# Kernel optimization log

Hardware: AMD Instinct MI355X
Metric: run time of the kernel (lower is better)

The kernel has to match this reference:

```python
import jax, jax.numpy as jnp
import numpy as np


def setup_inputs() -> dict:
    key = jax.random.key(0)
    ks = jax.random.split(key, 6)
    B, S, E, H = 8, 2048, 1024, 64
    scale = 1.0 / np.sqrt(E)
    return {
        "query": jax.random.normal(ks[0], (B, S, E), dtype=jnp.float32),
        "key": jax.random.normal(ks[1], (B, S, E), dtype=jnp.float32),
        "value": jax.random.normal(ks[2], (B, S, E), dtype=jnp.float32),
        "Wq": jax.random.normal(ks[3], (E, H), dtype=jnp.float32) * scale,
        "bq": jnp.zeros((H,), dtype=jnp.float32),
        "Wk": jax.random.normal(ks[4], (E, H), dtype=jnp.float32) * scale,
        "bk": jnp.zeros((H,), dtype=jnp.float32),
        "Wv": jax.random.normal(ks[5], (E, H), dtype=jnp.float32) * scale,
        "bv": jnp.zeros((H,), dtype=jnp.float32),
    }


def reference(query, key, value, Wq, bq, Wk, bk, Wv, bv):
    # Linear projections: [B,S,E] @ [E,H] + [H] -> [B,S,H]
    q = jnp.einsum("bse,eh->bsh", query, Wq) + bq
    k = jnp.einsum("bse,eh->bsh", key, Wk) + bk
    v = jnp.einsum("bse,eh->bsh", value, Wv) + bv
    head_dim = q.shape[-1]
    # scores [B,S,S], softmax over last axis, then weighted sum of values
    scores = jnp.einsum("bqh,bkh->bqk", q, k) / jnp.sqrt(
        jnp.asarray(head_dim, dtype=q.dtype)
    )
    attn = jax.nn.softmax(scores, axis=-1)
    return jnp.einsum("bqk,bkh->bqh", attn, v)
```

## Files before the change

### kernel.cpp

```cpp
#include <hip/hip_runtime.h>
#include <math.h>

#define BB 8
#define SS 2048
#define EE 1024
#define HH 64
#define MM (BB * SS)

typedef unsigned short u16;
typedef __attribute__((ext_vector_type(8))) short short8;
typedef __attribute__((ext_vector_type(4))) float floatx4;

__device__ __forceinline__ u16 f2bf(float f) {
    union { float f; unsigned u; } a; a.f = f;
    unsigned r = a.u + 0x7fffu + ((a.u >> 16) & 1u);
    return (u16)(r >> 16);
}

__device__ __forceinline__ void split2(float f0, float f1, unsigned& hp, unsigned& lp) {
    union { float f; unsigned u; } a0, a1, h0, h1, l0, l1;
    a0.f = f0; a1.f = f1;
    h0.u = a0.u & 0xffff0000u;
    h1.u = a1.u & 0xffff0000u;
    l0.f = f0 - h0.f;
    l1.f = f1 - h1.f;
    hp = __builtin_amdgcn_perm(a1.u, a0.u, 0x07060302u);
    lp = __builtin_amdgcn_perm(l1.u, l0.u, 0x07060302u);
}

__device__ __forceinline__ void async_copy16(const u16* g, u16* l) {
    __builtin_amdgcn_global_load_lds(
        (const __attribute__((address_space(1))) unsigned*)g,
        (__attribute__((address_space(3))) unsigned*)l, 16, 0, 0);
}

template <int CTRL>
__device__ __forceinline__ float dppf(float x) {
    union { float f; int i; } a, b;
    a.f = x;
    b.i = __builtin_amdgcn_update_dpp(a.i, a.i, CTRL, 0xF, 0xF, true);
    return b.f;
}
__device__ __forceinline__ float red_max16(float x) {
    x = fmaxf(x, dppf<0xB1>(x));
    x = fmaxf(x, dppf<0x4E>(x));
    x = fmaxf(x, dppf<0x141>(x));
    x = fmaxf(x, dppf<0x140>(x));
    return x;
}
__device__ __forceinline__ float red_sum16(float x) {
    x += dppf<0xB1>(x);
    x += dppf<0x4E>(x);
    x += dppf<0x141>(x);
    x += dppf<0x140>(x);
    return x;
}

#define WP_MAT 131072

__global__ __launch_bounds__(512) void pack_w(
    const float* __restrict__ W0, const float* __restrict__ W1, const float* __restrict__ W2,
    u16* __restrict__ Wp)
{
    const int which = blockIdx.y;
    const float* __restrict__ W = (which == 0) ? W0 : (which == 1) ? W1 : W2;
    const float scale = (which == 0) ? 0.125f : 1.0f;
    const int t    = blockIdx.x;
    const int tid  = threadIdx.x;
    const int ks   = tid >> 8;
    const int nt   = (tid >> 6) & 3;
    const int lane = tid & 63;
    const int n    = lane & 15;
    const int g    = lane >> 4;

    const int k0 = t * 64 + ks * 32 + g * 8;
    const int c  = nt * 16 + n;

    float e[8];
    #pragma unroll
    for (int j = 0; j < 8; ++j) e[j] = W[(size_t)(k0 + j) * HH + c] * scale;

    unsigned hp[4], lp[4];
    #pragma unroll
    for (int i = 0; i < 4; ++i) split2(e[2 * i], e[2 * i + 1], hp[i], lp[i]);

    u16* dst = Wp + (size_t)which * WP_MAT
                  + ((size_t)(t * 8 + ks * 4 + nt) * 2) * 512 + lane * 8;
    *(uint4*)dst         = (uint4){hp[0], hp[1], hp[2], hp[3]};
    *(uint4*)(dst + 512) = (uint4){lp[0], lp[1], lp[2], lp[3]};
}

#define PCH 16

#define LOAD_A(AV, T)                                   \
    {                                                   \
        const float* p_ = ap + (T) * 64;                \
        AV[0] = *(const float4*)(p_ + 0);               \
        AV[1] = *(const float4*)(p_ + 4);               \
        AV[2] = *(const float4*)(p_ + 32);              \
        AV[3] = *(const float4*)(p_ + 36);              \
    }

#define STAGE_W(TSTAGE, SBUF)                                                  \
    {                                                                          \
        const u16* src_ = wpb + (size_t)(TSTAGE) * 8192 + wave * 2048 + lane * 8; \
        u16* dst_ = &Wb[SBUF][wave * 2048];                                    \
        async_copy16(src_ + 0 * 512, dst_ + 0 * 512);                          \
        async_copy16(src_ + 1 * 512, dst_ + 1 * 512);                          \
        async_copy16(src_ + 2 * 512, dst_ + 2 * 512);                          \
        async_copy16(src_ + 3 * 512, dst_ + 3 * 512);                          \
    }

#define VBARN(N)                                                    \
    {                                                               \
        __builtin_amdgcn_sched_barrier(0);                          \
        asm volatile("s_waitcnt vmcnt(" #N ")" ::: "memory");       \
        __builtin_amdgcn_s_barrier();                               \
        __builtin_amdgcn_sched_barrier(0);                          \
    }

#define PROJ_CHUNK(AV, WBUF, SBUF, TSTAGE, TPREF)                                  \
    {                                                                              \
        if ((TSTAGE) < PCH) STAGE_W(TSTAGE, SBUF);                                 \
        __builtin_amdgcn_sched_barrier(0);                                         \
        short8 ah0, ah1, al0, al1;                                                 \
        {                                                                          \
            unsigned hp0, lp0, hp1, lp1, hp2, lp2, hp3, lp3;                       \
            split2(AV[0].x, AV[0].y, hp0, lp0);                                    \
            split2(AV[0].z, AV[0].w, hp1, lp1);                                    \
            split2(AV[1].x, AV[1].y, hp2, lp2);                                    \
            split2(AV[1].z, AV[1].w, hp3, lp3);                                    \
            union { uint4 u; short8 s; } ch_, cl_;                                 \
            ch_.u = (uint4){hp0, hp1, hp2, hp3};                                   \
            cl_.u = (uint4){lp0, lp1, lp2, lp3};                                   \
            ah0 = ch_.s; al0 = cl_.s;                                              \
            split2(AV[2].x, AV[2].y, hp0, lp0);                                    \
            split2(AV[2].z, AV[2].w, hp1, lp1);                                    \
            split2(AV[3].x, AV[3].y, hp2, lp2);                                    \
            split2(AV[3].z, AV[3].w, hp3, lp3);                                    \
            ch_.u = (uint4){hp0, hp1, hp2, hp3};                                   \
            cl_.u = (uint4){lp0, lp1, lp2, lp3};                                   \
            ah1 = ch_.s; al1 = cl_.s;                                              \
        }                                                                          \
        if ((TPREF) < PCH) LOAD_A(AV, TPREF);                                      \
        _Pragma("unroll")                                                          \
        for (int nt = 0; nt < 4; ++nt) {                                           \
            const short8 whf = *(const short8*)&Wb[WBUF][nt * 1024 + lane * 8];    \
            const short8 wlf = *(const short8*)&Wb[WBUF][nt * 1024 + 512 + lane * 8]; \
            acc[nt] = __builtin_amdgcn_mfma_f32_16x16x32_bf16(ah0, whf, acc[nt], 0, 0, 0); \
            acc[nt] = __builtin_amdgcn_mfma_f32_16x16x32_bf16(al0, whf, acc[nt], 0, 0, 0); \
            acc[nt] = __builtin_amdgcn_mfma_f32_16x16x32_bf16(ah0, wlf, acc[nt], 0, 0, 0); \
        }                                                                          \
        _Pragma("unroll")                                                          \
        for (int nt = 0; nt < 4; ++nt) {                                           \
            const short8 whf = *(const short8*)&Wb[WBUF][4096 + nt * 1024 + lane * 8]; \
            const short8 wlf = *(const short8*)&Wb[WBUF][4096 + nt * 1024 + 512 + lane * 8]; \
            acc[nt] = __builtin_amdgcn_mfma_f32_16x16x32_bf16(ah1, whf, acc[nt], 0, 0, 0); \
            acc[nt] = __builtin_amdgcn_mfma_f32_16x16x32_bf16(al1, whf, acc[nt], 0, 0, 0); \
            acc[nt] = __builtin_amdgcn_mfma_f32_16x16x32_bf16(ah1, wlf, acc[nt], 0, 0, 0); \
        }                                                                          \
    }

__global__ __launch_bounds__(256) void proj_mfma(
    const float* __restrict__ A0, const float* __restrict__ A1, const float* __restrict__ A2,
    const u16* __restrict__ Wp,
    const float* __restrict__ b0, const float* __restrict__ b1, const float* __restrict__ b2,
    u16* __restrict__ o0, u16* __restrict__ o1, u16* __restrict__ o2)
{
    const int which = blockIdx.y;
    const float* __restrict__ A    = (which == 0) ? A0 : (which == 1) ? A1 : A2;
    const float* __restrict__ bias = (which == 0) ? b0 : (which == 1) ? b1 : b2;
    u16* __restrict__ out          = (which == 0) ? o0 : (which == 1) ? o1 : o2;
    const float bscale = (which == 0) ? 0.125f : 1.0f;

    __shared__ __align__(16) u16 Wb[3][8192];

    const int tid  = threadIdx.x;
    const int lane = tid & 63;
    const int wave = tid >> 6;
    const int n    = lane & 15;
    const int g    = lane >> 4;
    const int row0 = blockIdx.x * 64;

    const float* __restrict__ ap = A + (size_t)(row0 + wave * 16 + n) * EE + g * 8;
    const u16* __restrict__ wpb = Wp + (size_t)which * WP_MAT;

    floatx4 acc[4];
    #pragma unroll
    for (int nt = 0; nt < 4; ++nt) acc[nt] = (floatx4){0.f, 0.f, 0.f, 0.f};

    float4 avA[4], avB[4], avC[4];
    STAGE_W(0, 0);
    __builtin_amdgcn_sched_barrier(0);
    LOAD_A(avA, 0);
    LOAD_A(avB, 1);
    LOAD_A(avC, 2);
    __builtin_amdgcn_sched_barrier(0);
    STAGE_W(1, 1);
    VBARN(12);

    PROJ_CHUNK(avA, 0, 2, 2, 3);
    VBARN(8);

    for (int tt = 1; tt <= 10; tt += 3) {
        PROJ_CHUNK(avB, 1, 0, tt + 2, tt + 3);  VBARN(12);
        PROJ_CHUNK(avC, 2, 1, tt + 3, tt + 4);  VBARN(12);
        PROJ_CHUNK(avA, 0, 2, tt + 4, tt + 5);  VBARN(12);
    }

    PROJ_CHUNK(avB, 1, 0, 15, 16);
    VBARN(8);
    PROJ_CHUNK(avC, 2, 0, 16, 17);
    VBARN(0);
    PROJ_CHUNK(avA, 0, 0, 16, 17);

    #pragma unroll
    for (int nt = 0; nt < 4; ++nt) {
        const float bv = bias[nt * 16 + n] * bscale;
        #pragma unroll
        for (int r = 0; r < 4; ++r) {
            const int row = row0 + wave * 16 + g * 4 + r;
            out[(size_t)row * HH + nt * 16 + n] = f2bf(acc[nt][r] + bv);
        }
    }
}

__global__ __launch_bounds__(256) void flash_mfma(
    const u16* __restrict__ qp, const u16* __restrict__ kp,
    const u16* __restrict__ vp, float* __restrict__ out)
{
    __shared__ __align__(16) u16 Ks[2][64 * 64];
    __shared__ __align__(16) u16 Vt[2][64 * 64];
    __shared__ __align__(16) u16 Pw[4][16 * 72];

    const int b    = blockIdx.y;
    const int q0   = blockIdx.x * 32;
    const int tid  = threadIdx.x;
    const int lane = tid & 63;
    const int wave = tid >> 6;
    const int wq   = wave & 1;
    const int ks   = wave >> 1;
    const int n    = lane & 15;
    const int g    = lane >> 4;

    const u16* qrow = qp + ((size_t)b * SS + q0 + wq * 16 + n) * HH;
    const short8 qa0 = *(const short8*)(qrow + g * 8);
    const short8 qa1 = *(const short8*)(qrow + 32 + g * 8);

    floatx4 Oa[4];
    #pragma unroll
    for (int ht = 0; ht < 4; ++ht) Oa[ht] = (floatx4){0.f, 0.f, 0.f, 0.f};
    float m_i[4], l_ln[4];
    #pragma unroll
    for (int r = 0; r < 4; ++r) { m_i[r] = -1e30f; l_ln[r] = 0.f; }

    const u16* kb = kp + (size_t)b * SS * HH;
    const u16* vb = vp + (size_t)b * SS * HH;

    const int jK0 = tid >> 3, jK1 = 32 + (tid >> 3), cs = tid & 7;
    const int jV  = (tid & 15) * 4, hV = (tid >> 4) * 4;

    short8  kr0, kr1;
    ushort4 vr0, vr1, vr2, vr3;

    kr0 = *(const short8*)(kb + (size_t)jK0 * HH + cs * 8);
    kr1 = *(const short8*)(kb + (size_t)jK1 * HH + cs * 8);
    vr0 = *(const ushort4*)(vb + (size_t)(jV + 0) * HH + hV);
    vr1 = *(const ushort4*)(vb + (size_t)(jV + 1) * HH + hV);
    vr2 = *(const ushort4*)(vb + (size_t)(jV + 2) * HH + hV);
    vr3 = *(const ushort4*)(vb + (size_t)(jV + 3) * HH + hV);
    {
        *(short8*)&Ks[0][jK0 * 64 + ((cs ^ (jK0 & 7)) << 3)] = kr0;
        *(short8*)&Ks[0][jK1 * 64 + ((cs ^ (jK1 & 7)) << 3)] = kr1;
        const u16* a0 = (const u16*)&vr0; const u16* a1 = (const u16*)&vr1;
        const u16* a2 = (const u16*)&vr2; const u16* a3 = (const u16*)&vr3;
        #pragma unroll
        for (int i = 0; i < 4; ++i) {
            const int h = hV + i;
            ushort4 w; w.x = a0[i]; w.y = a1[i]; w.z = a2[i]; w.w = a3[i];
            *(ushort4*)((char*)&Vt[0][0] + h * 128 + (((jV >> 3) ^ (h & 7)) << 4) + ((jV & 4) << 1)) = w;
        }
    }
    __syncthreads();

    for (int t = 0; t < SS / 64; ++t) {
        const int cur = t & 1;

        if (t + 1 < SS / 64) {
            const size_t kt = (size_t)(t + 1) * 64;
            kr0 = *(const short8*)(kb + (kt + jK0) * HH + cs * 8);
            kr1 = *(const short8*)(kb + (kt + jK1) * HH + cs * 8);
            vr0 = *(const ushort4*)(vb + (kt + jV + 0) * HH + hV);
            vr1 = *(const ushort4*)(vb + (kt + jV + 1) * HH + hV);
            vr2 = *(const ushort4*)(vb + (kt + jV + 2) * HH + hV);
            vr3 = *(const ushort4*)(vb + (kt + jV + 3) * HH + hV);
        }

        floatx4 S[2];
        #pragma unroll
        for (int nt = 0; nt < 2; ++nt) {
            const int j = ks * 32 + nt * 16 + n;
            const short8 kf0 = *(const short8*)&Ks[cur][j * 64 + (((0 + g) ^ (j & 7)) << 3)];
            const short8 kf1 = *(const short8*)&Ks[cur][j * 64 + (((4 + g) ^ (j & 7)) << 3)];
            floatx4 a = (floatx4){0.f, 0.f, 0.f, 0.f};
            __builtin_amdgcn_s_setprio(1);
            a = __builtin_amdgcn_mfma_f32_16x16x32_bf16(qa0, kf0, a, 0, 0, 0);
            a = __builtin_amdgcn_mfma_f32_16x16x32_bf16(qa1, kf1, a, 0, 0, 0);
            __builtin_amdgcn_s_setprio(0);
            S[nt] = a;
        }

        float mx[4];
        #pragma unroll
        for (int r = 0; r < 4; ++r)
            mx[r] = red_max16(fmaxf(S[0][r], S[1][r]));

        float alpha[4];
        #pragma unroll
        for (int r = 0; r < 4; ++r) {
            const float Mn = fmaxf(m_i[r], mx[r]);
            alpha[r] = __expf(m_i[r] - Mn);
            m_i[r]   = Mn;
        }
        float p[2][4];
        #pragma unroll
        for (int nt = 0; nt < 2; ++nt)
            #pragma unroll
            for (int r = 0; r < 4; ++r)
                p[nt][r] = __expf(S[nt][r] - m_i[r]);
        #pragma unroll
        for (int r = 0; r < 4; ++r)
            l_ln[r] = l_ln[r] * alpha[r] + (p[0][r] + p[1][r]);
        #pragma unroll
        for (int ht = 0; ht < 4; ++ht)
            #pragma unroll
            for (int r = 0; r < 4; ++r) Oa[ht][r] *= alpha[r];

        #pragma unroll
        for (int nt = 0; nt < 2; ++nt)
            #pragma unroll
            for (int r = 0; r < 4; ++r)
                Pw[wave][(g * 4 + r) * 72 + nt * 16 + n] = f2bf(p[nt][r]);
        const short8 pa = *(const short8*)&Pw[wave][n * 72 + g * 8];

        __builtin_amdgcn_s_setprio(1);
        #pragma unroll
        for (int ht = 0; ht < 4; ++ht) {
            const int h = ht * 16 + n;
            const short8 vf = *(const short8*)((const char*)&Vt[cur][0] + h * 128 +
                                               ((((ks << 2) + g) ^ (h & 7)) << 4));
            Oa[ht] = __builtin_amdgcn_mfma_f32_16x16x32_bf16(pa, vf, Oa[ht], 0, 0, 0);
        }
        __builtin_amdgcn_s_setprio(0);

        if (t + 1 < SS / 64) {
            const int nx = cur ^ 1;
            *(short8*)&Ks[nx][jK0 * 64 + ((cs ^ (jK0 & 7)) << 3)] = kr0;
            *(short8*)&Ks[nx][jK1 * 64 + ((cs ^ (jK1 & 7)) << 3)] = kr1;
            const u16* a0 = (const u16*)&vr0; const u16* a1 = (const u16*)&vr1;
            const u16* a2 = (const u16*)&vr2; const u16* a3 = (const u16*)&vr3;
            #pragma unroll
            for (int i = 0; i < 4; ++i) {
                const int h = hV + i;
                ushort4 w; w.x = a0[i]; w.y = a1[i]; w.z = a2[i]; w.w = a3[i];
                *(ushort4*)((char*)&Vt[nx][0] + h * 128 + (((jV >> 3) ^ (h & 7)) << 4) + ((jV & 4) << 1)) = w;
            }
        }
        __syncthreads();
    }

    float l_i[4];
    #pragma unroll
    for (int r = 0; r < 4; ++r) l_i[r] = red_sum16(l_ln[r]);

    float* Cb = (float*)&Ks[0][0];
    float* Cm = Cb + 2 * 16 * 68;
    float* Cl = Cm + 32;
    if (ks == 1) {
        #pragma unroll
        for (int ht = 0; ht < 4; ++ht)
            #pragma unroll
            for (int r = 0; r < 4; ++r)
                Cb[(wq * 16 + g * 4 + r) * 68 + ht * 16 + n] = Oa[ht][r];
        if (n == 0)
            #pragma unroll
            for (int r = 0; r < 4; ++r) {
                Cm[wq * 16 + g * 4 + r] = m_i[r];
                Cl[wq * 16 + g * 4 + r] = l_i[r];
            }
    }
    __syncthreads();
    if (ks == 0) {
        float a0v[4], a1v[4], linv[4];
        #pragma unroll
        for (int r = 0; r < 4; ++r) {
            const int m = g * 4 + r;
            const float m1 = Cm[wq * 16 + m], l1 = Cl[wq * 16 + m];
            const float M  = fmaxf(m_i[r], m1);
            const float e0 = __expf(m_i[r] - M), e1 = __expf(m1 - M);
            a0v[r] = e0; a1v[r] = e1;
            linv[r] = 1.f / (l_i[r] * e0 + l1 * e1);
        }
        #pragma unroll
        for (int ht = 0; ht < 4; ++ht)
            #pragma unroll
            for (int r = 0; r < 4; ++r) {
                const float o1 = Cb[(wq * 16 + g * 4 + r) * 68 + ht * 16 + n];
                const float v  = (Oa[ht][r] * a0v[r] + o1 * a1v[r]) * linv[r];
                out[((size_t)b * SS + q0 + wq * 16 + g * 4 + r) * HH + ht * 16 + n] = v;
            }
    }
}

extern "C" void kernel_launch(void* const* d_in, const int* in_sizes, int n_in,
                              void* d_out, int out_size, void* d_ws, size_t ws_size,
                              hipStream_t stream) {
    const float* query = (const float*)d_in[0];
    const float* key   = (const float*)d_in[1];
    const float* value = (const float*)d_in[2];
    const float* Wq    = (const float*)d_in[3];
    const float* bq    = (const float*)d_in[4];
    const float* Wk    = (const float*)d_in[5];
    const float* bk    = (const float*)d_in[6];
    const float* Wv    = (const float*)d_in[7];
    const float* bv    = (const float*)d_in[8];
    float* out = (float*)d_out;

    u16* qp = (u16*)d_ws;
    u16* kp = qp + (size_t)MM * HH;
    u16* vp = kp + (size_t)MM * HH;
    u16* Wp = vp + (size_t)MM * HH;

    dim3 wgrid(EE / 64, 3);
    pack_w<<<wgrid, 512, 0, stream>>>(Wq, Wk, Wv, Wp);

    dim3 pgrid(MM / 64, 3);
    proj_mfma<<<pgrid, 256, 0, stream>>>(query, key, value,
                                         Wp,
                                         bq, bk, bv,
                                         qp, kp, vp);

    dim3 agrid(SS / 32, BB);
    flash_mfma<<<agrid, 256, 0, stream>>>(qp, kp, vp, out);
}
```

Baseline: 258.0 us.

## Stage projection A tiles through LDS with coalesced loads and double buffering

The projection kernel used to load A directly into MFMA fragment layout with strided per-lane float4 reads and a hand-tuned triple-buffered vmcnt pipeline. Now each wave loads 16 rows with fully coalesced row-contiguous reads into registers, writes them to a padded LDS tile, and reads fragments back from LDS. W staging drops to double buffering, with plain __syncthreads between chunks. This aims for better global-load coalescing, at the cost of extra LDS traffic, a full block barrier per chunk, and a shallower prefetch depth.

```diff
diff --git a/kernel.cpp b/kernel.cpp
--- a/kernel.cpp
+++ b/kernel.cpp
@@ -92,15 +92,6 @@
 
 #define PCH 16
 
-#define LOAD_A(AV, T)                                   \
-    {                                                   \
-        const float* p_ = ap + (T) * 64;                \
-        AV[0] = *(const float4*)(p_ + 0);               \
-        AV[1] = *(const float4*)(p_ + 4);               \
-        AV[2] = *(const float4*)(p_ + 32);              \
-        AV[3] = *(const float4*)(p_ + 36);              \
-    }
-
 #define STAGE_W(TSTAGE, SBUF)                                                  \
     {                                                                          \
         const u16* src_ = wpb + (size_t)(TSTAGE) * 8192 + wave * 2048 + lane * 8; \
@@ -111,54 +102,68 @@
         async_copy16(src_ + 3 * 512, dst_ + 3 * 512);                          \
     }
 
-#define VBARN(N)                                                    \
-    {                                                               \
-        __builtin_amdgcn_sched_barrier(0);                          \
-        asm volatile("s_waitcnt vmcnt(" #N ")" ::: "memory");       \
-        __builtin_amdgcn_s_barrier();                               \
-        __builtin_amdgcn_sched_barrier(0);                          \
-    }
-
-#define PROJ_CHUNK(AV, WBUF, SBUF, TSTAGE, TPREF)                                  \
+#define LOAD_A_REGS(RA, T)                                                     \
+    _Pragma("unroll")                                                          \
+    for (int j = 0; j < 16; ++j)                                               \
+        RA[j] = apw[(size_t)j * EE + (T) * 64 + lane];
+
+#define WRITE_A_LDS(RA, BUF)                                                   \
+    _Pragma("unroll")                                                          \
+    for (int j = 0; j < 16; ++j)                                               \
+        Alds[BUF][wave][j * 66 + lane] = RA[j];
+
+#define PROJ_CHUNK(CUR, TNEXT)                                                     \
     {                                                                              \
-        if ((TSTAGE) < PCH) STAGE_W(TSTAGE, SBUF);                                 \
-        __builtin_amdgcn_sched_barrier(0);                                         \
+        if ((TNEXT) < PCH) {                                                       \
+            STAGE_W(TNEXT, (CUR) ^ 1);                                             \
+            LOAD_A_REGS(rA, TNEXT);                                                \
+        }                                                                          \
+        const float* ab = &Alds[CUR][wave][n * 66];                                \
         short8 ah0, ah1, al0, al1;                                                 \
         {                                                                          \
+            const float2 e0 = *(const float2*)(ab + g * 8 + 0);                    \
+            const float2 e1 = *(const float2*)(ab + g * 8 + 2);                    \
+            const float2 e2 = *(const float2*)(ab + g * 8 + 4);                    \
+            const float2 e3 = *(const float2*)(ab + g * 8 + 6);                    \
+            const float2 f0 = *(const float2*)(ab + 32 + g * 8 + 0);               \
+            const float2 f1 = *(const float2*)(ab + 32 + g * 8 + 2);               \
+            const float2 f2 = *(const float2*)(ab + 32 + g * 8 + 4);               \
+            const float2 f3 = *(const float2*)(ab + 32 + g * 8 + 6);               \
             unsigned hp0, lp0, hp1, lp1, hp2, lp2, hp3, lp3;                       \
-            split2(AV[0].x, AV[0].y, hp0, lp0);                                    \
-            split2(AV[0].z, AV[0].w, hp1, lp1);                                    \
-            split2(AV[1].x, AV[1].y, hp2, lp2);                                    \
-            split2(AV[1].z, AV[1].w, hp3, lp3);                                    \
+            split2(e0.x, e0.y, hp0, lp0);                                          \
+            split2(e1.x, e1.y, hp1, lp1);                                          \
+            split2(e2.x, e2.y, hp2, lp2);                                          \
+            split2(e3.x, e3.y, hp3, lp3);                                          \
             union { uint4 u; short8 s; } ch_, cl_;                                 \
             ch_.u = (uint4){hp0, hp1, hp2, hp3};                                   \
             cl_.u = (uint4){lp0, lp1, lp2, lp3};                                   \
             ah0 = ch_.s; al0 = cl_.s;                                              \
-            split2(AV[2].x, AV[2].y, hp0, lp0);                                    \
-            split2(AV[2].z, AV[2].w, hp1, lp1);                                    \
-            split2(AV[3].x, AV[3].y, hp2, lp2);                                    \
-            split2(AV[3].z, AV[3].w, hp3, lp3);                                    \
+            split2(f0.x, f0.y, hp0, lp0);                                          \
+            split2(f1.x, f1.y, hp1, lp1);                                          \
+            split2(f2.x, f2.y, hp2, lp2);                                          \
+            split2(f3.x, f3.y, hp3, lp3);                                          \
             ch_.u = (uint4){hp0, hp1, hp2, hp3};                                   \
             cl_.u = (uint4){lp0, lp1, lp2, lp3};                                   \
             ah1 = ch_.s; al1 = cl_.s;                                              \
         }                                                                          \
-        if ((TPREF) < PCH) LOAD_A(AV, TPREF);                                      \
         _Pragma("unroll")                                                          \
         for (int nt = 0; nt < 4; ++nt) {                                           \
-            const short8 whf = *(const short8*)&Wb[WBUF][nt * 1024 + lane * 8];    \
-            const short8 wlf = *(const short8*)&Wb[WBUF][nt * 1024 + 512 + lane * 8]; \
+            const short8 whf = *(const short8*)&Wb[CUR][nt * 1024 + lane * 8];     \
+            const short8 wlf = *(const short8*)&Wb[CUR][nt * 1024 + 512 + lane * 8]; \
             acc[nt] = __builtin_amdgcn_mfma_f32_16x16x32_bf16(ah0, whf, acc[nt], 0, 0, 0); \
             acc[nt] = __builtin_amdgcn_mfma_f32_16x16x32_bf16(al0, whf, acc[nt], 0, 0, 0); \
             acc[nt] = __builtin_amdgcn_mfma_f32_16x16x32_bf16(ah0, wlf, acc[nt], 0, 0, 0); \
         }                                                                          \
         _Pragma("unroll")                                                          \
         for (int nt = 0; nt < 4; ++nt) {                                           \
-            const short8 whf = *(const short8*)&Wb[WBUF][4096 + nt * 1024 + lane * 8]; \
-            const short8 wlf = *(const short8*)&Wb[WBUF][4096 + nt * 1024 + 512 + lane * 8]; \
+            const short8 whf = *(const short8*)&Wb[CUR][4096 + nt * 1024 + lane * 8]; \
+            const short8 wlf = *(const short8*)&Wb[CUR][4096 + nt * 1024 + 512 + lane * 8]; \
             acc[nt] = __builtin_amdgcn_mfma_f32_16x16x32_bf16(ah1, whf, acc[nt], 0, 0, 0); \
             acc[nt] = __builtin_amdgcn_mfma_f32_16x16x32_bf16(al1, whf, acc[nt], 0, 0, 0); \
             acc[nt] = __builtin_amdgcn_mfma_f32_16x16x32_bf16(ah1, wlf, acc[nt], 0, 0, 0); \
         }                                                                          \
+        if ((TNEXT) < PCH) WRITE_A_LDS(rA, (CUR) ^ 1);                             \
+        __syncthreads();                                                           \
     }
 
 __global__ __launch_bounds__(256) void proj_mfma(
@@ -173,7 +178,8 @@
     u16* __restrict__ out          = (which == 0) ? o0 : (which == 1) ? o1 : o2;
     const float bscale = (which == 0) ? 0.125f : 1.0f;
 
-    __shared__ __align__(16) u16 Wb[3][8192];
+    __shared__ __align__(16) u16 Wb[2][8192];
+    __shared__ __align__(16) float Alds[2][4][16 * 66];
 
     const int tid  = threadIdx.x;
     const int lane = tid & 63;
@@ -182,37 +188,24 @@
     const int g    = lane >> 4;
     const int row0 = blockIdx.x * 64;
 
-    const float* __restrict__ ap = A + (size_t)(row0 + wave * 16 + n) * EE + g * 8;
+    const float* __restrict__ apw = A + (size_t)(row0 + wave * 16) * EE;
     const u16* __restrict__ wpb = Wp + (size_t)which * WP_MAT;
 
     floatx4 acc[4];
     #pragma unroll
     for (int nt = 0; nt < 4; ++nt) acc[nt] = (floatx4){0.f, 0.f, 0.f, 0.f};
 
-    float4 avA[4], avB[4], avC[4];
+    float rA[16];
+
     STAGE_W(0, 0);
-    __builtin_amdgcn_sched_barrier(0);
-    LOAD_A(avA, 0);
-    LOAD_A(avB, 1);
-    LOAD_A(avC, 2);
-    __builtin_amdgcn_sched_barrier(0);
-    STAGE_W(1, 1);
-    VBARN(12);
-
-    PROJ_CHUNK(avA, 0, 2, 2, 3);
-    VBARN(8);
-
-    for (int tt = 1; tt <= 10; tt += 3) {
-        PROJ_CHUNK(avB, 1, 0, tt + 2, tt + 3);  VBARN(12);
-        PROJ_CHUNK(avC, 2, 1, tt + 3, tt + 4);  VBARN(12);
-        PROJ_CHUNK(avA, 0, 2, tt + 4, tt + 5);  VBARN(12);
-    }
-
-    PROJ_CHUNK(avB, 1, 0, 15, 16);
-    VBARN(8);
-    PROJ_CHUNK(avC, 2, 0, 16, 17);
-    VBARN(0);
-    PROJ_CHUNK(avA, 0, 0, 16, 17);
+    LOAD_A_REGS(rA, 0);
+    WRITE_A_LDS(rA, 0);
+    __syncthreads();
+
+    for (int tt = 0; tt < PCH; tt += 2) {
+        PROJ_CHUNK(0, tt + 1);
+        PROJ_CHUNK(1, tt + 2);
+    }
 
     #pragma unroll
     for (int nt = 0; nt < 4; ++nt) {
```

Result: slower. 270.6 us (+4.9%).
